# Kernel tuning notes

Hardware: AMD Instinct MI355X
Metric: run time of the kernel (lower is better)

Reference implementation:

```python
import jax, jax.numpy as jnp
import numpy as np

WS = 8          # window size
HEADS = 6
DIM = 192


def _rel_idx(ws):
    # index [q, k] -> flat relative-position index into table of size (2ws-1)^2
    pos = jnp.arange(ws * ws)
    ph, pw = pos // ws, pos % ws
    rel_h = ph[None, :] - ph[:, None] + ws - 1  # k_h - q_h + ws - 1
    rel_w = pw[None, :] - pw[:, None] + ws - 1
    return rel_h * (2 * ws - 1) + rel_w  # [ws*ws, ws*ws]


def setup_inputs() -> dict:
    key = jax.random.key(0)
    ks = jax.random.split(key, 4)
    x = jax.random.normal(ks[0], (4, DIM, 256, 256), jnp.float32)
    qkv_w = jax.random.normal(ks[1], (3 * DIM, DIM), jnp.float32) * 0.02  # 1x1 conv
    qkv_b = jnp.zeros((3 * DIM,), jnp.float32)
    out_w = jax.random.normal(ks[2], (DIM, DIM), jnp.float32) * 0.02      # 1x1 conv
    out_b = jnp.zeros((DIM,), jnp.float32)
    rpe_table = jax.random.normal(ks[3], (HEADS, (2 * WS - 1) ** 2), jnp.float32) * 0.001
    return {"x": x, "qkv_w": qkv_w, "qkv_b": qkv_b,
            "out_w": out_w, "out_b": out_b, "rpe_table": rpe_table}


def reference(x, qkv_w, qkv_b, out_w, out_b, rpe_table):
    B, C, H, W = x.shape
    ws, heads = WS, HEADS
    hd, wd = H // ws, W // ws          # H,W chosen divisible by ws -> pad is no-op
    c = C // heads                     # head dim
    n = ws * ws                        # tokens per window

    # 1x1 conv to qkv
    qkv = jnp.einsum('bchw,oc->bohw', x, qkv_w) + qkv_b[None, :, None, None]
    # feat_to_win: b (3 heads c) (hd ws) (wd ws) -> 3, (b hd wd), heads, n, c
    qkv = qkv.reshape(B, 3, heads, c, hd, ws, wd, ws)
    qkv = qkv.transpose(1, 0, 4, 6, 2, 5, 7, 3).reshape(3, B * hd * wd, heads, n, c)
    q, k, v = qkv[0], qkv[1], qkv[2]

    bias = rpe_table[:, _rel_idx(ws)]  # [heads, n, n]
    scale = c ** -0.5
    scores = jnp.einsum('whqc,whkc->whqk', q, k) * scale + bias[None]
    attn = jax.nn.softmax(scores, axis=-1)
    out = jnp.einsum('whqk,whkc->whqc', attn, v)

    # win_to_feat: (b hd wd) heads n c -> b (heads c) H W
    out = out.reshape(B, hd, wd, heads, ws, ws, c)
    out = out.transpose(0, 3, 6, 1, 4, 2, 5).reshape(B, C, H, W)

    out = jnp.einsum('bchw,oc->bohw', out, out_w) + out_b[None, :, None, None]
    return out
```

## Files before the change

### kernel.cpp

```cpp
#include <hip/hip_runtime.h>
#include <cstdint>
#include <cstddef>

typedef __attribute__((ext_vector_type(8))) short short8;
typedef __attribute__((ext_vector_type(4))) float floatx4;

#define SEG 50331648ull

__device__ __forceinline__ unsigned short bf16rne(float f) {
  union { float f; unsigned int u; } c; c.f = f;
  unsigned int u = c.u;
  return (unsigned short)((u + 0x7fffu + ((u >> 16) & 1u)) >> 16);
}
__device__ __forceinline__ unsigned int packbf(float a, float b) {
  return (unsigned int)bf16rne(a) | ((unsigned int)bf16rne(b) << 16);
}

__global__ __launch_bounds__(256) void x_to_bf16(const float* __restrict__ x,
                                                 unsigned short* __restrict__ xb) {
  __shared__ float Tl[64][65];
  const int tid = threadIdx.x;
  const int ptile = blockIdx.x, cc = blockIdx.y, b = blockIdx.z;
  const float* src = x + ((size_t)(b * 192 + cc * 64)) * 65536 + ptile * 64;
  {
    int row = tid >> 2;
    int cb = (tid & 3) * 4;
#pragma unroll
    for (int rr = 0; rr < 4; ++rr) {
      int col = cb + rr * 16;
      float4 v = *(const float4*)(src + (size_t)row * 65536 + col);
      *(float4*)&Tl[row][col] = v;
    }
  }
  __syncthreads();
  unsigned short* dst = xb + ((size_t)b * 65536 + (size_t)ptile * 64) * 192 + cc * 64;
  {
    int p_l = tid >> 2;
    int c0 = (tid & 3) * 16;
    unsigned int w[8];
#pragma unroll
    for (int e = 0; e < 8; ++e)
      w[e] = packbf(Tl[c0 + 2 * e][p_l], Tl[c0 + 2 * e + 1][p_l]);
    *(uint4*)(dst + (size_t)p_l * 192 + c0)     = make_uint4(w[0], w[1], w[2], w[3]);
    *(uint4*)(dst + (size_t)p_l * 192 + c0 + 8) = make_uint4(w[4], w[5], w[6], w[7]);
  }
}

__global__ void bias_prep(const float* __restrict__ rpe, float* __restrict__ bias_d) {
  const int head = blockIdx.x;
  const int tid = threadIdx.x;
  for (int e = tid; e < 1024; e += 256) {
    int it = e >> 8, jt = (e >> 6) & 3, ln = e & 63;
    int quad = ln >> 4, n = ln & 15;
    int j = jt * 16 + n;
    int jh = j >> 3, jw = j & 7;
    float4 out;
    float* o = (float*)&out;
#pragma unroll
    for (int r = 0; r < 4; ++r) {
      int m = it * 16 + quad * 4 + r;
      int idx = (jh - (m >> 3) + 7) * 15 + (jw - (m & 7) + 7);
      o[r] = rpe[head * 225 + idx];
    }
    *(float4*)(bias_d + ((size_t)(head * 16 + it * 4 + jt) * 64 + ln) * 4) = out;
  }
}

#define WPAD 200
#define XPAD 40
__global__ __launch_bounds__(256) void qkv_mm(
    const unsigned short* __restrict__ xb, const float* __restrict__ wq,
    const float* __restrict__ qkv_b,
    unsigned short* __restrict__ q, unsigned short* __restrict__ k,
    unsigned short* __restrict__ v) {
  __shared__ unsigned short Wl[64 * WPAD];
  __shared__ unsigned short Xl[256 * XPAD];
  const int tid = threadIdx.x;
  const int ot = blockIdx.x, pt = blockIdx.y, b = blockIdx.z;
  const int o0 = ot * 64;
  {
    int o = tid >> 2, cb = (tid & 3) * 4;
    const float* wr = wq + (size_t)(o0 + o) * 192;
#pragma unroll
    for (int r = 0; r < 12; ++r) {
      int c = cb + r * 16;
      float4 wv = *(const float4*)(wr + c);
      *(uint2*)&Wl[o * WPAD + c] = make_uint2(packbf(wv.x, wv.y), packbf(wv.z, wv.w));
    }
  }
  const int lane = tid & 63, w = tid >> 6;
  const int n16 = lane & 15, quad = lane >> 4;
  floatx4 acc[4][4];
  const floatx4 fz = {0.f, 0.f, 0.f, 0.f};
#pragma unroll
  for (int i = 0; i < 4; ++i)
#pragma unroll
    for (int j = 0; j < 4; ++j) acc[i][j] = fz;

  const unsigned short* xrow = xb + ((size_t)b * 65536 + (size_t)pt * 256) * 192;
  for (int k0 = 0; k0 < 192; k0 += 32) {
#pragma unroll
    for (int pass = 0; pass < 4; ++pass) {
      int p_l = pass * 64 + (tid >> 2);
      int ch = tid & 3;
      short8 xv = *(const short8*)(xrow + (size_t)p_l * 192 + k0 + ch * 8);
      *(short8*)&Xl[p_l * XPAD + ch * 8] = xv;
    }
    __syncthreads();
    short8 a[4], bf[4];
#pragma unroll
    for (int i = 0; i < 4; ++i)
      a[i] = *(const short8*)&Wl[(16 * i + n16) * WPAD + k0 + quad * 8];
#pragma unroll
    for (int j = 0; j < 4; ++j)
      bf[j] = *(const short8*)&Xl[(w * 64 + 16 * j + n16) * XPAD + quad * 8];
#pragma unroll
    for (int i = 0; i < 4; ++i)
#pragma unroll
      for (int j = 0; j < 4; ++j)
        acc[i][j] = __builtin_amdgcn_mfma_f32_16x16x32_bf16(a[i], bf[j], acc[i][j], 0, 0, 0);
    __syncthreads();
  }
  const int sel = ot / 3;
  unsigned short* dst = (sel == 0) ? q : ((sel == 1) ? k : v);
  const float scl = (sel == 0) ? 0.17677669529663687f : 1.0f;
  const int hwin = pt >> 3, hin = pt & 7;
#pragma unroll
  for (int j = 0; j < 4; ++j) {
    int wcol = w * 64 + 16 * j + n16;
    int win = (b << 10) + hwin * 32 + (wcol >> 3);
    int t = hin * 8 + (wcol & 7);
#pragma unroll
    for (int i = 0; i < 4; ++i) {
      int og = o0 + 16 * i + quad * 4;
      int off = og - sel * 192;
      int head = off >> 5, c = off & 31;
      float4 bb = *(const float4*)(qkv_b + og);
      float v0 = (acc[i][j][0] + bb.x) * scl;
      float v1 = (acc[i][j][1] + bb.y) * scl;
      float v2 = (acc[i][j][2] + bb.z) * scl;
      float v3 = (acc[i][j][3] + bb.w) * scl;
      *(uint2*)(dst + ((size_t)(win * 6 + head) * 64 + t) * 32 + c) =
          make_uint2(packbf(v0, v1), packbf(v2, v3));
    }
  }
}

__global__ __launch_bounds__(256) void attn(
    const unsigned short* __restrict__ q, const unsigned short* __restrict__ k,
    const unsigned short* __restrict__ v, const float* __restrict__ bias_d,
    unsigned short* __restrict__ AO) {
  __shared__ unsigned short pl[4][64 * 72];
  __shared__ unsigned short vl[4][32 * 72];
  const int tid = threadIdx.x, w = tid >> 6, lane = tid & 63;
  const int n16 = lane & 15, quad = lane >> 4;
  const int wh = blockIdx.x * 4 + w;
  const int win = wh / 6, head = wh - win * 6;
  const unsigned short* qb = q + (size_t)wh * 2048;
  const unsigned short* kb = k + (size_t)wh * 2048;
  const unsigned short* vb = v + (size_t)wh * 2048;

  short8 vrow[4];
#pragma unroll
  for (int c8 = 0; c8 < 4; ++c8)
    vrow[c8] = *(const short8*)(vb + lane * 32 + c8 * 8);

  short8 aq[4], bk[4];
#pragma unroll
  for (int it = 0; it < 4; ++it)
    aq[it] = *(const short8*)(qb + (16 * it + n16) * 32 + quad * 8);
#pragma unroll
  for (int jt = 0; jt < 4; ++jt)
    bk[jt] = *(const short8*)(kb + (16 * jt + n16) * 32 + quad * 8);

  unsigned short* vlw = (unsigned short*)vl[w];
#pragma unroll
  for (int c8 = 0; c8 < 4; ++c8)
#pragma unroll
    for (int e = 0; e < 8; ++e)
      vlw[(c8 * 8 + e) * 72 + lane] = (unsigned short)vrow[c8][e];

  floatx4 s[4][4];
  const floatx4 fz = {0.f, 0.f, 0.f, 0.f};
#pragma unroll
  for (int it = 0; it < 4; ++it)
#pragma unroll
    for (int jt = 0; jt < 4; ++jt)
      s[it][jt] = __builtin_amdgcn_mfma_f32_16x16x32_bf16(aq[it], bk[jt], fz, 0, 0, 0);

  const float* bD = bias_d + (size_t)head * 4096;
  unsigned short* plw = (unsigned short*)pl[w];
#pragma unroll
  for (int it = 0; it < 4; ++it) {
    floatx4 bb[4];
#pragma unroll
    for (int jt = 0; jt < 4; ++jt)
      bb[jt] = *(const floatx4*)(bD + ((size_t)(it * 4 + jt) * 64 + lane) * 4);
#pragma unroll
    for (int r = 0; r < 4; ++r) {
      float x0 = s[it][0][r] + bb[0][r];
      float x1 = s[it][1][r] + bb[1][r];
      float x2 = s[it][2][r] + bb[2][r];
      float x3 = s[it][3][r] + bb[3][r];
      float m = fmaxf(fmaxf(x0, x1), fmaxf(x2, x3));
      m = fmaxf(m, __shfl_xor(m, 1));
      m = fmaxf(m, __shfl_xor(m, 2));
      m = fmaxf(m, __shfl_xor(m, 4));
      m = fmaxf(m, __shfl_xor(m, 8));
      float e0 = __expf(x0 - m), e1 = __expf(x1 - m);
      float e2 = __expf(x2 - m), e3 = __expf(x3 - m);
      float sum = e0 + e1 + e2 + e3;
      sum += __shfl_xor(sum, 1);
      sum += __shfl_xor(sum, 2);
      sum += __shfl_xor(sum, 4);
      sum += __shfl_xor(sum, 8);
      float inv = 1.0f / sum;
      int mr = it * 16 + quad * 4 + r;
      plw[mr * 72 + 0 * 16 + n16] = bf16rne(e0 * inv);
      plw[mr * 72 + 1 * 16 + n16] = bf16rne(e1 * inv);
      plw[mr * 72 + 2 * 16 + n16] = bf16rne(e2 * inv);
      plw[mr * 72 + 3 * 16 + n16] = bf16rne(e3 * inv);
    }
  }

  short8 bv[2][2], ap[4][2];
#pragma unroll
  for (int ct = 0; ct < 2; ++ct)
#pragma unroll
    for (int kk = 0; kk < 2; ++kk)
      bv[ct][kk] = *(const short8*)&vlw[(16 * ct + n16) * 72 + kk * 32 + quad * 8];
#pragma unroll
  for (int it = 0; it < 4; ++it)
#pragma unroll
    for (int kk = 0; kk < 2; ++kk)
      ap[it][kk] = *(const short8*)&plw[(16 * it + n16) * 72 + kk * 32 + quad * 8];
  floatx4 o[4][2];
#pragma unroll
  for (int it = 0; it < 4; ++it)
#pragma unroll
    for (int ct = 0; ct < 2; ++ct) {
      floatx4 acc = __builtin_amdgcn_mfma_f32_16x16x32_bf16(ap[it][0], bv[ct][0], fz, 0, 0, 0);
      o[it][ct] = __builtin_amdgcn_mfma_f32_16x16x32_bf16(ap[it][1], bv[ct][1], acc, 0, 0, 0);
    }

  unsigned short* ol = plw;
#pragma unroll
  for (int it = 0; it < 4; ++it)
#pragma unroll
    for (int ct = 0; ct < 2; ++ct)
#pragma unroll
      for (int r = 0; r < 4; ++r)
        ol[(16 * it + quad * 4 + r) * 40 + 16 * ct + n16] = bf16rne(o[it][ct][r]);

  const int t = lane;
  const int bimg = win >> 10, rem = win & 1023;
  const int h0 = (rem >> 5) << 3, w0 = (rem & 31) << 3;
  const size_t pix = ((size_t)bimg << 16) + (size_t)(h0 + (t >> 3)) * 256 + w0 + (t & 7);
  unsigned short* dstp = AO + pix * 192 + head * 32;
#pragma unroll
  for (int c8 = 0; c8 < 4; ++c8)
    *(short8*)(dstp + c8 * 8) = *(const short8*)&ol[t * 40 + c8 * 8];
}

__global__ __launch_bounds__(256) void out_mm(
    const unsigned short* __restrict__ AO, const float* __restrict__ w2,
    const float* __restrict__ b2, float* __restrict__ out) {
  __shared__ unsigned short Wl[64 * WPAD];
  __shared__ unsigned short Xl[256 * XPAD];
  const int tid = threadIdx.x;
  const int ox = blockIdx.x, pt = blockIdx.y, b = blockIdx.z;
  const int o0 = ox * 64;
  {
    int o = tid >> 2, cb = (tid & 3) * 4;
    const float* wr = w2 + (size_t)(o0 + o) * 192;
#pragma unroll
    for (int r = 0; r < 12; ++r) {
      int c = cb + r * 16;
      float4 wv = *(const float4*)(wr + c);
      *(uint2*)&Wl[o * WPAD + c] = make_uint2(packbf(wv.x, wv.y), packbf(wv.z, wv.w));
    }
  }
  const int lane = tid & 63, w = tid >> 6;
  const int n16 = lane & 15, quad = lane >> 4;
  floatx4 acc[4][4];
  const floatx4 fz = {0.f, 0.f, 0.f, 0.f};
#pragma unroll
  for (int i = 0; i < 4; ++i)
#pragma unroll
    for (int j = 0; j < 4; ++j) acc[i][j] = fz;

  const unsigned short* arow = AO + ((size_t)b * 65536 + (size_t)pt * 256) * 192;
  for (int k0 = 0; k0 < 192; k0 += 32) {
#pragma unroll
    for (int pass = 0; pass < 4; ++pass) {
      int p_l = pass * 64 + (tid >> 2);
      int ch = tid & 3;
      short8 xv = *(const short8*)(arow + (size_t)p_l * 192 + k0 + ch * 8);
      *(short8*)&Xl[p_l * XPAD + ch * 8] = xv;
    }
    __syncthreads();
    short8 a[4], bf[4];
#pragma unroll
    for (int i = 0; i < 4; ++i)
      a[i] = *(const short8*)&Xl[(w * 64 + 16 * i + n16) * XPAD + quad * 8];
#pragma unroll
    for (int j = 0; j < 4; ++j)
      bf[j] = *(const short8*)&Wl[(16 * j + n16) * WPAD + k0 + quad * 8];
#pragma unroll
    for (int i = 0; i < 4; ++i)
#pragma unroll
      for (int j = 0; j < 4; ++j)
        acc[i][j] = __builtin_amdgcn_mfma_f32_16x16x32_bf16(a[i], bf[j], acc[i][j], 0, 0, 0);
    __syncthreads();
  }
#pragma unroll
  for (int j = 0; j < 4; ++j) {
    int o = o0 + 16 * j + n16;
    float bj = b2[o];
    float* obase = out + ((size_t)b * 192 + o) * 65536 + (size_t)pt * 256;
#pragma unroll
    for (int i = 0; i < 4; ++i) {
      int p = w * 64 + 16 * i + quad * 4;
      *(float4*)(obase + p) = make_float4(acc[i][j][0] + bj, acc[i][j][1] + bj,
                                          acc[i][j][2] + bj, acc[i][j][3] + bj);
    }
  }
}

extern "C" void kernel_launch(void* const* d_in, const int* in_sizes, int n_in,
                              void* d_out, int out_size, void* d_ws, size_t ws_size,
                              hipStream_t stream) {
  const float* x     = (const float*)d_in[0];
  const float* qkv_w = (const float*)d_in[1];
  const float* qkv_b = (const float*)d_in[2];
  const float* out_w = (const float*)d_in[3];
  const float* out_b = (const float*)d_in[4];
  const float* rpe   = (const float*)d_in[5];
  float* out = (float*)d_out;

  unsigned short* xb = (unsigned short*)d_ws;
  unsigned short* q  = xb + SEG;
  unsigned short* k  = q + SEG;
  unsigned short* v  = k + SEG;
  unsigned short* AO = v + SEG;
  float* bias_d = (float*)(AO + SEG);

  x_to_bf16<<<dim3(1024, 3, 4), 256, 0, stream>>>(x, xb);
  bias_prep<<<6, 256, 0, stream>>>(rpe, bias_d);
  qkv_mm<<<dim3(9, 256, 4), 256, 0, stream>>>(xb, qkv_w, qkv_b, q, k, v);
  attn<<<6144, 256, 0, stream>>>(q, k, v, bias_d, AO);
  out_mm<<<dim3(3, 256, 4), 256, 0, stream>>>(AO, out_w, out_b, out);
}
```

Baseline: 755.0 us.

## Keep activation tile resident in LDS and loop over output-channel tiles

Both 1x1-conv GEMMs now load a 128-pixel by full-K activation tile into shared memory once per block and iterate over all output-channel tiles inside the block. The next weight tile is prefetched into registers while MFMAs run on the current one. This removes the repeated global reads of activations across output-tile blocks (previously 9 or 3 blocks each re-read the same pixels). The trade-offs are fewer blocks (2048), more LDS per block, and serialized output tiles within a block.

```diff
diff --git a/kernel.cpp b/kernel.cpp
--- a/kernel.cpp
+++ b/kernel.cpp
@@ -66,82 +66,100 @@
   }
 }
 
-#define WPAD 200
-#define XPAD 40
+#define WP 200
+#define XP 200
 __global__ __launch_bounds__(256) void qkv_mm(
     const unsigned short* __restrict__ xb, const float* __restrict__ wq,
     const float* __restrict__ qkv_b,
     unsigned short* __restrict__ q, unsigned short* __restrict__ k,
     unsigned short* __restrict__ v) {
-  __shared__ unsigned short Wl[64 * WPAD];
-  __shared__ unsigned short Xl[256 * XPAD];
+  __shared__ unsigned short Xl[128 * XP];
+  __shared__ unsigned short Wl[64 * WP];
   const int tid = threadIdx.x;
-  const int ot = blockIdx.x, pt = blockIdx.y, b = blockIdx.z;
-  const int o0 = ot * 64;
-  {
-    int o = tid >> 2, cb = (tid & 3) * 4;
-    const float* wr = wq + (size_t)(o0 + o) * 192;
-#pragma unroll
-    for (int r = 0; r < 12; ++r) {
-      int c = cb + r * 16;
-      float4 wv = *(const float4*)(wr + c);
-      *(uint2*)&Wl[o * WPAD + c] = make_uint2(packbf(wv.x, wv.y), packbf(wv.z, wv.w));
-    }
-  }
+  const int pt = blockIdx.x, b = blockIdx.y;
   const int lane = tid & 63, w = tid >> 6;
   const int n16 = lane & 15, quad = lane >> 4;
-  floatx4 acc[4][4];
+
+  const unsigned short* xrow = xb + ((size_t)b * 65536 + (size_t)pt * 128) * 192;
+#pragma unroll
+  for (int r = 0; r < 12; ++r) {
+    int c = tid + 256 * r;
+    int row = c / 24;
+    int col = (c - row * 24) * 8;
+    short8 xv = *(const short8*)(xrow + (size_t)c * 8);
+    *(short8*)&Xl[row * XP + col] = xv;
+  }
+  const int wo = tid >> 2, wcb = (tid & 3) * 4;
+  float4 wpre[12];
+#pragma unroll
+  for (int r = 0; r < 12; ++r)
+    wpre[r] = *(const float4*)(wq + (size_t)wo * 192 + wcb + r * 16);
+#pragma unroll
+  for (int r = 0; r < 12; ++r)
+    *(uint2*)&Wl[wo * WP + wcb + r * 16] =
+        make_uint2(packbf(wpre[r].x, wpre[r].y), packbf(wpre[r].z, wpre[r].w));
+  __syncthreads();
+
   const floatx4 fz = {0.f, 0.f, 0.f, 0.f};
-#pragma unroll
-  for (int i = 0; i < 4; ++i)
-#pragma unroll
-    for (int j = 0; j < 4; ++j) acc[i][j] = fz;
-
-  const unsigned short* xrow = xb + ((size_t)b * 65536 + (size_t)pt * 256) * 192;
-  for (int k0 = 0; k0 < 192; k0 += 32) {
-#pragma unroll
-    for (int pass = 0; pass < 4; ++pass) {
-      int p_l = pass * 64 + (tid >> 2);
-      int ch = tid & 3;
-      short8 xv = *(const short8*)(xrow + (size_t)p_l * 192 + k0 + ch * 8);
-      *(short8*)&Xl[p_l * XPAD + ch * 8] = xv;
+#pragma unroll 1
+  for (int ot = 0; ot < 9; ++ot) {
+    if (ot < 8) {
+      const float* wr = wq + (size_t)((ot + 1) * 64 + wo) * 192 + wcb;
+#pragma unroll
+      for (int r = 0; r < 12; ++r) wpre[r] = *(const float4*)(wr + r * 16);
+    }
+    floatx4 acc[4][2];
+#pragma unroll
+    for (int i = 0; i < 4; ++i)
+#pragma unroll
+      for (int j = 0; j < 2; ++j) acc[i][j] = fz;
+#pragma unroll
+    for (int k0 = 0; k0 < 192; k0 += 32) {
+      short8 a[4], bf[2];
+#pragma unroll
+      for (int i = 0; i < 4; ++i)
+        a[i] = *(const short8*)&Wl[(16 * i + n16) * WP + k0 + quad * 8];
+#pragma unroll
+      for (int j = 0; j < 2; ++j)
+        bf[j] = *(const short8*)&Xl[(w * 32 + 16 * j + n16) * XP + k0 + quad * 8];
+#pragma unroll
+      for (int i = 0; i < 4; ++i)
+#pragma unroll
+        for (int j = 0; j < 2; ++j)
+          acc[i][j] = __builtin_amdgcn_mfma_f32_16x16x32_bf16(a[i], bf[j], acc[i][j], 0, 0, 0);
     }
     __syncthreads();
-    short8 a[4], bf[4];
-#pragma unroll
-    for (int i = 0; i < 4; ++i)
-      a[i] = *(const short8*)&Wl[(16 * i + n16) * WPAD + k0 + quad * 8];
-#pragma unroll
-    for (int j = 0; j < 4; ++j)
-      bf[j] = *(const short8*)&Xl[(w * 64 + 16 * j + n16) * XPAD + quad * 8];
-#pragma unroll
-    for (int i = 0; i < 4; ++i)
-#pragma unroll
-      for (int j = 0; j < 4; ++j)
-        acc[i][j] = __builtin_amdgcn_mfma_f32_16x16x32_bf16(a[i], bf[j], acc[i][j], 0, 0, 0);
+    if (ot < 8) {
+#pragma unroll
+      for (int r = 0; r < 12; ++r)
+        *(uint2*)&Wl[wo * WP + wcb + r * 16] =
+            make_uint2(packbf(wpre[r].x, wpre[r].y), packbf(wpre[r].z, wpre[r].w));
+    }
     __syncthreads();
-  }
-  const int sel = ot / 3;
-  unsigned short* dst = (sel == 0) ? q : ((sel == 1) ? k : v);
-  const float scl = (sel == 0) ? 0.17677669529663687f : 1.0f;
-  const int hwin = pt >> 3, hin = pt & 7;
-#pragma unroll
-  for (int j = 0; j < 4; ++j) {
-    int wcol = w * 64 + 16 * j + n16;
-    int win = (b << 10) + hwin * 32 + (wcol >> 3);
-    int t = hin * 8 + (wcol & 7);
-#pragma unroll
-    for (int i = 0; i < 4; ++i) {
-      int og = o0 + 16 * i + quad * 4;
-      int off = og - sel * 192;
-      int head = off >> 5, c = off & 31;
-      float4 bb = *(const float4*)(qkv_b + og);
-      float v0 = (acc[i][j][0] + bb.x) * scl;
-      float v1 = (acc[i][j][1] + bb.y) * scl;
-      float v2 = (acc[i][j][2] + bb.z) * scl;
-      float v3 = (acc[i][j][3] + bb.w) * scl;
-      *(uint2*)(dst + ((size_t)(win * 6 + head) * 64 + t) * 32 + c) =
-          make_uint2(packbf(v0, v1), packbf(v2, v3));
+
+    const int sel = ot / 3;
+    unsigned short* dst = (sel == 0) ? q : ((sel == 1) ? k : v);
+    const float scl = (sel == 0) ? 0.17677669529663687f : 1.0f;
+    const int h = pt >> 1;
+#pragma unroll
+    for (int j = 0; j < 2; ++j) {
+      int wcol = w * 32 + 16 * j + n16;
+      int wc = ((pt & 1) << 7) + wcol;
+      int win = (b << 10) + (h >> 3) * 32 + (wc >> 3);
+      int t = ((h & 7) << 3) + (wc & 7);
+#pragma unroll
+      for (int i = 0; i < 4; ++i) {
+        int og = ot * 64 + 16 * i + quad * 4;
+        int off = og - sel * 192;
+        int head = off >> 5, c = off & 31;
+        float4 bb = *(const float4*)(qkv_b + og);
+        float v0 = (acc[i][j][0] + bb.x) * scl;
+        float v1 = (acc[i][j][1] + bb.y) * scl;
+        float v2 = (acc[i][j][2] + bb.z) * scl;
+        float v3 = (acc[i][j][3] + bb.w) * scl;
+        *(uint2*)(dst + ((size_t)(win * 6 + head) * 64 + t) * 32 + c) =
+            make_uint2(packbf(v0, v1), packbf(v2, v3));
+      }
     }
   }
 }
@@ -265,64 +283,81 @@
 __global__ __launch_bounds__(256) void out_mm(
     const unsigned short* __restrict__ AO, const float* __restrict__ w2,
     const float* __restrict__ b2, float* __restrict__ out) {
-  __shared__ unsigned short Wl[64 * WPAD];
-  __shared__ unsigned short Xl[256 * XPAD];
+  __shared__ unsigned short Xl[128 * XP];
+  __shared__ unsigned short Wl[64 * WP];
   const int tid = threadIdx.x;
-  const int ox = blockIdx.x, pt = blockIdx.y, b = blockIdx.z;
-  const int o0 = ox * 64;
-  {
-    int o = tid >> 2, cb = (tid & 3) * 4;
-    const float* wr = w2 + (size_t)(o0 + o) * 192;
-#pragma unroll
-    for (int r = 0; r < 12; ++r) {
-      int c = cb + r * 16;
-      float4 wv = *(const float4*)(wr + c);
-      *(uint2*)&Wl[o * WPAD + c] = make_uint2(packbf(wv.x, wv.y), packbf(wv.z, wv.w));
-    }
-  }
+  const int pt = blockIdx.x, b = blockIdx.y;
   const int lane = tid & 63, w = tid >> 6;
   const int n16 = lane & 15, quad = lane >> 4;
-  floatx4 acc[4][4];
+
+  const unsigned short* arow = AO + ((size_t)b * 65536 + (size_t)pt * 128) * 192;
+#pragma unroll
+  for (int r = 0; r < 12; ++r) {
+    int c = tid + 256 * r;
+    int row = c / 24;
+    int col = (c - row * 24) * 8;
+    short8 xv = *(const short8*)(arow + (size_t)c * 8);
+    *(short8*)&Xl[row * XP + col] = xv;
+  }
+  const int wo = tid >> 2, wcb = (tid & 3) * 4;
+  float4 wpre[12];
+#pragma unroll
+  for (int r = 0; r < 12; ++r)
+    wpre[r] = *(const float4*)(w2 + (size_t)wo * 192 + wcb + r * 16);
+#pragma unroll
+  for (int r = 0; r < 12; ++r)
+    *(uint2*)&Wl[wo * WP + wcb + r * 16] =
+        make_uint2(packbf(wpre[r].x, wpre[r].y), packbf(wpre[r].z, wpre[r].w));
+  __syncthreads();
+
   const floatx4 fz = {0.f, 0.f, 0.f, 0.f};
-#pragma unroll
-  for (int i = 0; i < 4; ++i)
-#pragma unroll
-    for (int j = 0; j < 4; ++j) acc[i][j] = fz;
-
-  const unsigned short* arow = AO + ((size_t)b * 65536 + (size_t)pt * 256) * 192;
-  for (int k0 = 0; k0 < 192; k0 += 32) {
-#pragma unroll
-    for (int pass = 0; pass < 4; ++pass) {
-      int p_l = pass * 64 + (tid >> 2);
-      int ch = tid & 3;
-      short8 xv = *(const short8*)(arow + (size_t)p_l * 192 + k0 + ch * 8);
-      *(short8*)&Xl[p_l * XPAD + ch * 8] = xv;
+#pragma unroll 1
+  for (int ot = 0; ot < 3; ++ot) {
+    if (ot < 2) {
+      const float* wr = w2 + (size_t)((ot + 1) * 64 + wo) * 192 + wcb;
+#pragma unroll
+      for (int r = 0; r < 12; ++r) wpre[r] = *(const float4*)(wr + r * 16);
+    }
+    floatx4 acc[2][4];
+#pragma unroll
+    for (int i = 0; i < 2; ++i)
+#pragma unroll
+      for (int j = 0; j < 4; ++j) acc[i][j] = fz;
+#pragma unroll
+    for (int k0 = 0; k0 < 192; k0 += 32) {
+      short8 a[2], bf[4];
+#pragma unroll
+      for (int i = 0; i < 2; ++i)
+        a[i] = *(const short8*)&Xl[(w * 32 + 16 * i + n16) * XP + k0 + quad * 8];
+#pragma unroll
+      for (int j = 0; j < 4; ++j)
+        bf[j] = *(const short8*)&Wl[(16 * j + n16) * WP + k0 + quad * 8];
+#pragma unroll
+      for (int i = 0; i < 2; ++i)
+#pragma unroll
+        for (int j = 0; j < 4; ++j)
+          acc[i][j] = __builtin_amdgcn_mfma_f32_16x16x32_bf16(a[i], bf[j], acc[i][j], 0, 0, 0);
     }
     __syncthreads();
-    short8 a[4], bf[4];
-#pragma unroll
-    for (int i = 0; i < 4; ++i)
-      a[i] = *(const short8*)&Xl[(w * 64 + 16 * i + n16) * XPAD + quad * 8];
-#pragma unroll
-    for (int j = 0; j < 4; ++j)
-      bf[j] = *(const short8*)&Wl[(16 * j + n16) * WPAD + k0 + quad * 8];
-#pragma unroll
-    for (int i = 0; i < 4; ++i)
-#pragma unroll
-      for (int j = 0; j < 4; ++j)
-        acc[i][j] = __builtin_amdgcn_mfma_f32_16x16x32_bf16(a[i], bf[j], acc[i][j], 0, 0, 0);
+    if (ot < 2) {
+#pragma unroll
+      for (int r = 0; r < 12; ++r)
+        *(uint2*)&Wl[wo * WP + wcb + r * 16] =
+            make_uint2(packbf(wpre[r].x, wpre[r].y), packbf(wpre[r].z, wpre[r].w));
+    }
     __syncthreads();
-  }
-#pragma unroll
-  for (int j = 0; j < 4; ++j) {
-    int o = o0 + 16 * j + n16;
-    float bj = b2[o];
-    float* obase = out + ((size_t)b * 192 + o) * 65536 + (size_t)pt * 256;
-#pragma unroll
-    for (int i = 0; i < 4; ++i) {
-      int p = w * 64 + 16 * i + quad * 4;
-      *(float4*)(obase + p) = make_float4(acc[i][j][0] + bj, acc[i][j][1] + bj,
-                                          acc[i][j][2] + bj, acc[i][j][3] + bj);
+
+#pragma unroll
+    for (int j = 0; j < 4; ++j) {
+      int o = ot * 64 + 16 * j + n16;
+      float bj = b2[o];
+      float* obase = out + ((size_t)b * 192 + o) * 65536 + (size_t)pt * 128;
+#pragma unroll
+      for (int i = 0; i < 2; ++i) {
+        int p = w * 32 + 16 * i + quad * 4;
+        *(float4*)(obase + p) = make_float4(acc[i][j][0] + bj, acc[i][j][1] + bj,
+                                            acc[i][j][2] + bj, acc[i][j][3] + bj);
+      }
     }
   }
 }
@@ -347,7 +382,7 @@
 
   x_to_bf16<<<dim3(1024, 3, 4), 256, 0, stream>>>(x, xb);
   bias_prep<<<6, 256, 0, stream>>>(rpe, bias_d);
-  qkv_mm<<<dim3(9, 256, 4), 256, 0, stream>>>(xb, qkv_w, qkv_b, q, k, v);
+  qkv_mm<<<dim3(512, 4), 256, 0, stream>>>(xb, qkv_w, qkv_b, q, k, v);
   attn<<<6144, 256, 0, stream>>>(q, k, v, bias_d, AO);
-  out_mm<<<dim3(3, 256, 4), 256, 0, stream>>>(AO, out_w, out_b, out);
-}
+  out_mm<<<dim3(512, 4), 256, 0, stream>>>(AO, out_w, out_b, out);
+}
```

After: 678.5 us. 10.1% less time.
